# Kernel tuning notes

Measured on AMD Instinct MI355X. Metric: run time of the kernel, lower is better.

The kernel has to match this reference:

```python
import jax, jax.numpy as jnp
import numpy as np

B, CIN, H, W = 4, 256, 32, 32
COUT, DK, DV, NH = 256, 64, 64, 8
L = H * W
DKH = DK // NH
DVH = DV // NH
ALPHA, BETA = 0.5, 0.5
PAD = 1
LEAK = 0.01
GN_EPS = 1e-5


def conv2d(x, w, b=None, padding=0):
    out = jax.lax.conv_general_dilated(
        x, w, window_strides=(1, 1),
        padding=[(padding, padding), (padding, padding)],
        dimension_numbers=('NCHW', 'OIHW', 'NCHW'))
    if b is not None:
        out = out + b[None, :, None, None]
    return out


def rel_to_abs(x):
    # x: [B, Nh, L, 2L-1] -> [B, Nh, L, L]
    b, nh, l, _ = x.shape
    x = jnp.concatenate([x, jnp.zeros((b, nh, l, 1), x.dtype)], axis=3)
    flat = x.reshape(b, nh, l * 2 * l)
    flat = jnp.concatenate([flat, jnp.zeros((b, nh, l - 1), x.dtype)], axis=2)
    final = flat.reshape(b, nh, l + 1, 2 * l - 1)
    return final[:, :, :l, l - 1:]


def setup_inputs() -> dict:
    key = jax.random.key(0)
    ks = jax.random.split(key, 8)
    s = 0.02
    return {
        'x': jax.random.normal(ks[0], (B, CIN, H, W), jnp.float32),
        'prev_att': jax.random.normal(ks[1], (B, NH, L, L), jnp.float32) * 0.1,
        'conv_v': jax.random.normal(ks[2], (COUT - DV, CIN, 3, 3), jnp.float32) * s,
        'conv_g': jnp.ones((COUT - DV, 1, 1, 1), jnp.float32),
        'conv_b': jnp.zeros((COUT - DV,), jnp.float32),
        'qkv_w': jax.random.normal(ks[3], (2 * DK + DV, CIN, 1, 1), jnp.float32) * s,
        'qkv_b': jnp.zeros((2 * DK + DV,), jnp.float32),
        'attc_w': jax.random.normal(ks[4], (NH, NH, 3, 3), jnp.float32) * s,
        'attc_b': jnp.zeros((NH,), jnp.float32),
        'gn_w': jnp.ones((NH,), jnp.float32),
        'gn_b': jnp.zeros((NH,), jnp.float32),
        'rel_k': jax.random.normal(ks[5], (2 * L - 1, DKH), jnp.float32),
    }


def reference(x, prev_att, conv_v, conv_g, conv_b, qkv_w, qkv_b,
              attc_w, attc_b, gn_w, gn_b, rel_k):
    # ---- weight-normed conv branch (k < 1) ----
    vnorm = jnp.sqrt(jnp.sum(conv_v * conv_v, axis=(1, 2, 3), keepdims=True))
    w_eff = conv_g * conv_v / vnorm
    conv_out = conv2d(x, w_eff, conv_b, padding=PAD)
    conv_out = conv_out[:, :, :-PAD, :-PAD]  # Chomp2d

    # ---- attention branch (dk > 0, no downsample) ----
    qkv = conv2d(x, qkv_w, qkv_b, padding=0).reshape(B, 2 * DK + DV, L)
    q = qkv[:, :DK].reshape(B, NH, DKH, L) * (DKH ** -0.5)
    k = qkv[:, DK:2 * DK].reshape(B, NH, DKH, L)
    v = qkv[:, 2 * DK:].reshape(B, NH, DVH, L)

    logits = jnp.einsum('bhdl,bhdm->bhlm', q, k)  # [B,Nh,L,L]

    # relative position logits
    rel = jnp.einsum('bhld,md->bhlm', q.transpose(0, 1, 3, 2), rel_k)  # [B,Nh,L,2L-1]
    logits = logits + rel_to_abs(rel)

    # blend with previous attention + conv/GroupNorm refinement
    att_matrix = (1.0 - BETA) * logits + BETA * prev_att
    t = conv2d(att_matrix, attc_w, attc_b, padding=1)
    mu = jnp.mean(t, axis=(1, 2, 3), keepdims=True)
    var = jnp.var(t, axis=(1, 2, 3), keepdims=True)
    t = (t - mu) / jnp.sqrt(var + GN_EPS)
    t = t * gn_w[None, :, None, None] + gn_b[None, :, None, None]
    t = jnp.where(t >= 0, t, LEAK * t)  # LeakyReLU
    logits = ALPHA * t + (1.0 - ALPHA) * att_matrix

    weights = jax.nn.softmax(logits, axis=-1)
    attn = jnp.einsum('bhlm,bhmd->bhld', weights, v.transpose(0, 1, 3, 2))  # [B,Nh,L,dvh]
    # faithful to torch: reshape (not transpose) [B,Nh,L,dvh] -> [B,Nh,dvh,L]
    attn = attn.reshape(B, NH, DVH, L).reshape(B, DV, H, W)
    attn = attn[:, :, :-PAD, :-PAD]  # Chomp2d

    out = jnp.concatenate([conv_out, attn], axis=1)  # [B, COUT, H-1, W-1]
    return (out, logits)
```

## Files before the change

kernel.cpp:

```cpp
#include <hip/hip_runtime.h>
#include <math.h>

#define NB   4
#define CINc 256
#define LLEN 1024
#define NHEAD 8
#define QKVOC 192
#define CONVOC 192
#define OHW  31

#define WS_SCALE 0
#define WS_STATS 192
#define WS_PART  256
#define WS_QKV   8448
#define WS_E     794880
#define WS_CPART 1057024

typedef __attribute__((ext_vector_type(8))) short bf16x8;
typedef __attribute__((ext_vector_type(4))) float f32x4;

__device__ __forceinline__ unsigned short f2bf(float f) {
    unsigned int u = __float_as_uint(f);
    u += 0x7FFFu + ((u >> 16) & 1u);
    return (unsigned short)(u >> 16);
}
__device__ __forceinline__ float bf2f(unsigned short s) {
    return __uint_as_float(((unsigned int)s) << 16);
}

__global__ void k_wnorm(const float* __restrict__ conv_v, const float* __restrict__ conv_g,
                        float* __restrict__ ws) {
    int o = blockIdx.x, t = threadIdx.x;
    const float* v = conv_v + (size_t)o * 2304;
    float s = 0.f;
    for (int i = t; i < 2304; i += 256) { float x = v[i]; s += x * x; }
    for (int off = 1; off < 64; off <<= 1) s += __shfl_xor(s, off, 64);
    __shared__ float red[4];
    if ((t & 63) == 0) red[t >> 6] = s;
    __syncthreads();
    if (t == 0) {
        float tot = red[0] + red[1] + red[2] + red[3];
        ws[WS_SCALE + o] = conv_g[o] / sqrtf(tot);
    }
}

__global__ __launch_bounds__(256) void k_qkv(const float* __restrict__ x,
                                             const float* __restrict__ qkv_w,
                                             const float* __restrict__ qkv_b,
                                             float* __restrict__ ws) {
    int og = blockIdx.x, b = blockIdx.y, t = threadIdx.x;
    int o0 = og * 4;
    const float* xb = x + (size_t)b * CINc * LLEN;
    float acc[4][4] = {};
    for (int c = 0; c < CINc; c++) {
        float xv[4];
#pragma unroll
        for (int k = 0; k < 4; k++) xv[k] = xb[(size_t)c * LLEN + t + 256 * k];
#pragma unroll
        for (int oo = 0; oo < 4; oo++) {
            float w = qkv_w[(size_t)(o0 + oo) * CINc + c];
#pragma unroll
            for (int k = 0; k < 4; k++) acc[oo][k] += w * xv[k];
        }
    }
#pragma unroll
    for (int oo = 0; oo < 4; oo++) {
        int o = o0 + oo;
        float bias = qkv_b[o];
        float sc = (o < 64) ? 0.35355339059327373f : 1.0f;
#pragma unroll
        for (int k = 0; k < 4; k++)
            ws[WS_QKV + ((size_t)b * QKVOC + o) * LLEN + t + 256 * k] = (acc[oo][k] + bias) * sc;
    }
}

__global__ __launch_bounds__(256) void k_conv(const float* __restrict__ x,
                                              const float* __restrict__ conv_v,
                                              float* __restrict__ ws) {
    int ot = blockIdx.x, z = blockIdx.y, bz = blockIdx.z, t = threadIdx.x;
    int b = bz >> 1, half = bz & 1;
    int o0 = ot * 16, c0 = z * 32, r0 = half * 16;
    __shared__ unsigned short aW[16 * 288];
    __shared__ unsigned short xS[18 * 34 * 36];

    for (int idx = t; idx < 4608; idx += 256) {
        int o = idx / 288, k = idx - o * 288;
        int tap = k >> 5, c = k & 31;
        aW[o * 288 + k] = f2bf(conv_v[((size_t)(o0 + o) * CINc + c0 + c) * 9 + tap]);
    }
    unsigned int* xSu = reinterpret_cast<unsigned int*>(xS);
    for (int i = t; i < 11016; i += 256) xSu[i] = 0u;
    __syncthreads();
    const float* xb = x + ((size_t)b * CINc + c0) * 1024;
    for (int task = t; task < 2304; task += 256) {
        int cp = task & 15;
        int rr = (task >> 4) % 18;
        int wc = task / 288;
        int gr = r0 - 1 + rr;
        int gw = wc * 4;
        if (gr >= 0 && gr < 32) {
            float4 va = *reinterpret_cast<const float4*>(&xb[(size_t)(2 * cp) * 1024 + gr * 32 + gw]);
            float4 vb = *reinterpret_cast<const float4*>(&xb[(size_t)(2 * cp + 1) * 1024 + gr * 32 + gw]);
            int base = (rr * 34 + gw + 1) * 36 + 2 * cp;
            float a0[4] = {va.x, va.y, va.z, va.w};
            float b0[4] = {vb.x, vb.y, vb.z, vb.w};
#pragma unroll
            for (int j = 0; j < 4; j++) {
                unsigned int pk = (unsigned int)f2bf(a0[j]) | ((unsigned int)f2bf(b0[j]) << 16);
                *reinterpret_cast<unsigned int*>(&xS[base + j * 36]) = pk;
            }
        }
    }
    __syncthreads();

    int lane = t & 63, w = t >> 6;
    int col = lane & 15, kb = lane >> 4;
    bf16x8 afr[9];
#pragma unroll
    for (int tap = 0; tap < 9; tap++)
        afr[tap] = *reinterpret_cast<const bf16x8*>(&aW[col * 288 + tap * 32 + kb * 8]);
    char* xb8 = reinterpret_cast<char*>(xS);
#pragma unroll
    for (int tt = 0; tt < 8; tt++) {
        int pt = w * 8 + tt;
        int hl = pt >> 1, w0 = (pt & 1) * 16;
        f32x4 acc = {0.f, 0.f, 0.f, 0.f};
        int pbase = (hl * 34 + w0 + col) * 72 + kb * 16;
#pragma unroll
        for (int tap = 0; tap < 9; tap++) {
            int di = tap / 3, dj = tap % 3;
            bf16x8 bfr = *reinterpret_cast<const bf16x8*>(xb8 + pbase + (di * 34 + dj) * 72);
            acc = __builtin_amdgcn_mfma_f32_16x16x32_bf16(afr[tap], bfr, acc, 0, 0, 0);
        }
        int px = (r0 + hl) * 32 + w0 + col;
#pragma unroll
        for (int r = 0; r < 4; r++) {
            int o = kb * 4 + r;
            ws[WS_CPART + ((size_t)(b * 8 + z) * CONVOC + o0 + o) * 1024 + px] = acc[r];
        }
    }
}

__global__ __launch_bounds__(256) void k_convred(const float* __restrict__ conv_b,
                                                 const float* __restrict__ ws,
                                                 float* __restrict__ out) {
    int o = blockIdx.x, b = blockIdx.y, t = threadIdx.x;
    float sc = ws[WS_SCALE + o], bi = conv_b[o];
    for (int px = t; px < 1024; px += 256) {
        float s = 0.f;
#pragma unroll
        for (int z = 0; z < 8; z++)
            s += ws[WS_CPART + ((size_t)(b * 8 + z) * CONVOC + o) * 1024 + px];
        int hh = px >> 5, ww = px & 31;
        if (hh < 31 && ww < 31)
            out[((size_t)(b * 256 + o) * 31 + hh) * 31 + ww] = sc * s + bi;
    }
}

__global__ __launch_bounds__(256, 3) void k_att(const float* __restrict__ ws_,
                                                const float* __restrict__ prev,
                                                const float* __restrict__ rel_k,
                                                unsigned short* __restrict__ attB) {
    int jt = blockIdx.x, it = blockIdx.y, bh = blockIdx.z;
    int b = bh >> 3, h = bh & 7;
    int t = threadIdx.x;
    int i0 = it * 32, j0 = jt * 128;
    int ig = t >> 5, tj = t & 31;

    float4 pv[4];
    size_t poff = (((size_t)bh * 1024 + i0 + ig * 4) << 10) + j0 + tj * 4;
#pragma unroll
    for (int ii = 0; ii < 4; ii++)
        pv[ii] = *reinterpret_cast<const float4*>(&prev[poff + ((size_t)ii << 10)]);
    const float* rbase = rel_k + (size_t)(j0 - i0 + 1020 + 4 * (tj - ig)) * 8;
    float4 ra[7], rb[7];
#pragma unroll
    for (int dgi = 0; dgi < 7; dgi++) {
        ra[dgi] = *reinterpret_cast<const float4*>(rbase + dgi * 8);
        rb[dgi] = *reinterpret_cast<const float4*>(rbase + dgi * 8 + 4);
    }

    __shared__ float kS[8][128];
    __shared__ float qS[32][8];
    const float* qkv = ws_ + WS_QKV;
    const float* qplane = qkv + ((size_t)b * QKVOC + h * 8) * LLEN;
    const float* kplane = qkv + ((size_t)b * QKVOC + 64 + h * 8) * LLEN;
    {
        int d = t >> 5, jc = (t & 31) * 4;
        *reinterpret_cast<float4*>(&kS[d][jc]) =
            *reinterpret_cast<const float4*>(&kplane[(size_t)d * LLEN + j0 + jc]);
    }
    {
        int i = t >> 3, d = t & 7;
        qS[i][d] = qplane[(size_t)d * LLEN + i0 + i];
    }
    __syncthreads();

    float qr[4][8];
#pragma unroll
    for (int ii = 0; ii < 4; ii++) {
        float4 a = *reinterpret_cast<const float4*>(&qS[ig * 4 + ii][0]);
        float4 c = *reinterpret_cast<const float4*>(&qS[ig * 4 + ii][4]);
        qr[ii][0] = a.x; qr[ii][1] = a.y; qr[ii][2] = a.z; qr[ii][3] = a.w;
        qr[ii][4] = c.x; qr[ii][5] = c.y; qr[ii][6] = c.z; qr[ii][7] = c.w;
    }
    float acc[4][4] = {};
#pragma unroll
    for (int d = 0; d < 8; d++) {
        float4 kv = *reinterpret_cast<const float4*>(&kS[d][tj * 4]);
#pragma unroll
        for (int ii = 0; ii < 4; ii++) {
            float qv = qr[ii][d];
            acc[ii][0] += qv * kv.x; acc[ii][1] += qv * kv.y;
            acc[ii][2] += qv * kv.z; acc[ii][3] += qv * kv.w;
        }
    }
#pragma unroll
    for (int dgi = 0; dgi < 7; dgi++) {
#pragma unroll
        for (int ii = 0; ii < 4; ii++) {
#pragma unroll
            for (int jj = 0; jj < 4; jj++) {
                if (jj - ii + 3 == dgi) {
                    acc[ii][jj] += qr[ii][0] * ra[dgi].x + qr[ii][1] * ra[dgi].y
                                 + qr[ii][2] * ra[dgi].z + qr[ii][3] * ra[dgi].w
                                 + qr[ii][4] * rb[dgi].x + qr[ii][5] * rb[dgi].y
                                 + qr[ii][6] * rb[dgi].z + qr[ii][7] * rb[dgi].w;
                }
            }
        }
    }
#pragma unroll
    for (int ii = 0; ii < 4; ii++) {
        int i = i0 + ig * 4 + ii;
        size_t off = (((size_t)bh * 1024 + i) << 10) + j0 + tj * 4;
        ushort4 o16;
        o16.x = f2bf(0.5f * acc[ii][0] + 0.5f * pv[ii].x);
        o16.y = f2bf(0.5f * acc[ii][1] + 0.5f * pv[ii].y);
        o16.z = f2bf(0.5f * acc[ii][2] + 0.5f * pv[ii].z);
        o16.w = f2bf(0.5f * acc[ii][3] + 0.5f * pv[ii].w);
        *reinterpret_cast<ushort4*>(&attB[off]) = o16;
    }
}

__global__ __launch_bounds__(256) void k_attconv(const unsigned short* __restrict__ attB,
                                                 const float* __restrict__ attc_w,
                                                 const float* __restrict__ attc_b,
                                                 unsigned short* __restrict__ tB,
                                                 float* __restrict__ ws) {
    int jt = blockIdx.x, it = blockIdx.y, b = blockIdx.z, t = threadIdx.x;
    int i0 = it * 16, j0 = jt * 64;
    __shared__ unsigned short aW[16 * 96];
    __shared__ unsigned short xT[18 * 81 * 8];
    unsigned int* xU = reinterpret_cast<unsigned int*>(xT);

    for (int idx = t; idx < 1536; idx += 256) {
        int ho = idx / 96, k = idx - ho * 96;
        int tap = k >> 3, hp = k & 7;
        float w = (ho < 8 && tap < 9) ? attc_w[ho * 72 + hp * 9 + tap] : 0.f;
        aW[ho * 96 + k] = f2bf(w);
    }
    const unsigned short* attb = attB + (((size_t)b * 8) << 20);
    for (int task = t; task < 720; task += 256) {
        int r   = task % 18;
        int hpp = (task / 18) & 3;
        int ch  = task / 72;
        int gr  = i0 - 1 + r;
        int gc0 = j0 - 8 + ch * 8;
        uint4 va = make_uint4(0u, 0u, 0u, 0u), vb = va;
        if (gr >= 0 && gr < 1024 && gc0 >= 0 && gc0 < 1024) {
            size_t base = (((size_t)(hpp * 2)) << 20) + ((size_t)gr << 10) + gc0;
            va = *reinterpret_cast<const uint4*>(&attb[base]);
            vb = *reinterpret_cast<const uint4*>(&attb[base + (1u << 20)]);
        }
        int cbase = (r * 81 + ch * 8) * 4 + hpp;
        unsigned int aw[4] = {va.x, va.y, va.z, va.w};
        unsigned int bw[4] = {vb.x, vb.y, vb.z, vb.w};
#pragma unroll
        for (int q = 0; q < 4; q++) {
            xU[cbase + (2 * q) * 4]     = (aw[q] & 0xffffu) | (bw[q] << 16);
            xU[cbase + (2 * q + 1) * 4] = (aw[q] >> 16) | (bw[q] & 0xffff0000u);
        }
    }
    __syncthreads();

    int lane = t & 63, w = t >> 6;
    int col = lane & 15, kb = lane >> 4;
    bf16x8 afr[3];
#pragma unroll
    for (int c = 0; c < 3; c++)
        afr[c] = *reinterpret_cast<const bf16x8*>(&aW[col * 96 + c * 32 + kb * 8]);
    int offs[3];
#pragma unroll
    for (int c = 0; c < 3; c++) {
        int tap = c * 4 + kb;
        int di = (tap < 9) ? tap / 3 : 1;
        int dj = (tap < 9) ? tap % 3 : 1;
        offs[c] = (di * 81 + col + dj + 7) * 16;
    }
    float bias_r[4];
#pragma unroll
    for (int r = 0; r < 4; r++) {
        int ho = kb * 4 + r;
        bias_r[r] = (ho < 8) ? attc_b[ho] : 0.f;
    }
    float ssum = 0.f, ssq = 0.f;
    char* xbyte = reinterpret_cast<char*>(xT);
#pragma unroll
    for (int ri = 0; ri < 4; ri++) {
        int il = w * 4 + ri;
#pragma unroll
        for (int jg = 0; jg < 4; jg++) {
            f32x4 acc = {0.f, 0.f, 0.f, 0.f};
            int base = (il * 81 + jg * 16) * 16;
#pragma unroll
            for (int c = 0; c < 3; c++) {
                bf16x8 bfr = *reinterpret_cast<const bf16x8*>(xbyte + base + offs[c]);
                acc = __builtin_amdgcn_mfma_f32_16x16x32_bf16(afr[c], bfr, acc, 0, 0, 0);
            }
#pragma unroll
            for (int r = 0; r < 4; r++) {
                float v = acc[r] + bias_r[r];
                ssum += v; ssq += v * v;
                int ho = kb * 4 + r;
                if (ho < 8) {
                    size_t off = (((size_t)(b * 8 + ho)) << 20) + ((size_t)(i0 + il) << 10)
                               + j0 + jg * 16 + col;
                    tB[off] = f2bf(v);
                }
            }
        }
    }
    for (int off = 1; off < 64; off <<= 1) {
        ssum += __shfl_xor(ssum, off, 64);
        ssq  += __shfl_xor(ssq, off, 64);
    }
    __shared__ float r1[4], r2[4];
    if ((t & 63) == 0) { r1[t >> 6] = ssum; r2[t >> 6] = ssq; }
    __syncthreads();
    if (t == 0) {
        int lin = (b * 64 + it) * 16 + jt;
        ws[WS_PART + lin * 2]     = r1[0] + r1[1] + r1[2] + r1[3];
        ws[WS_PART + lin * 2 + 1] = r2[0] + r2[1] + r2[2] + r2[3];
    }
}

__global__ void k_stats(float* __restrict__ ws) {
    int b = blockIdx.x, t = threadIdx.x;
    float S = 0.f, Q = 0.f;
    for (int n = t; n < 1024; n += 256) {
        S += ws[WS_PART + (size_t)(b * 1024 + n) * 2];
        Q += ws[WS_PART + (size_t)(b * 1024 + n) * 2 + 1];
    }
    for (int off = 1; off < 64; off <<= 1) { S += __shfl_xor(S, off, 64); Q += __shfl_xor(Q, off, 64); }
    __shared__ float r1[4], r2[4];
    if ((t & 63) == 0) { r1[t >> 6] = S; r2[t >> 6] = Q; }
    __syncthreads();
    if (t == 0) {
        float Sa = r1[0] + r1[1] + r1[2] + r1[3];
        float Qa = r2[0] + r2[1] + r2[2] + r2[3];
        float N = 8.0f * 1024.f * 1024.f;
        float mean = Sa / N;
        float var = Qa / N - mean * mean;
        ws[WS_STATS + b * 2]     = mean;
        ws[WS_STATS + b * 2 + 1] = 1.0f / sqrtf(var + 1e-5f);
    }
}

__global__ __launch_bounds__(256) void k_final(const unsigned short* __restrict__ tB,
                                               const unsigned short* __restrict__ attB,
                                               float* __restrict__ logits,
                                               const float* __restrict__ gn_w,
                                               const float* __restrict__ gn_b,
                                               float* __restrict__ ws) {
    int row0 = blockIdx.x * 4;
    int b = row0 >> 13, h = (row0 >> 10) & 7;
    int t = threadIdx.x;
    float mean = ws[WS_STATS + b * 2], rstd = ws[WS_STATS + b * 2 + 1];
    float gwr = gn_w[h] * rstd;
    float gbm = gn_b[h] - mean * gwr;
    __shared__ float p[4][1024];
    __shared__ float red2[4][4];
    size_t base = (size_t)row0 * 1024 + t * 4;
    ushort4 tv[4], av[4];
#pragma unroll
    for (int r = 0; r < 4; r++) {
        tv[r] = *reinterpret_cast<const ushort4*>(&tB[base + (size_t)r * 1024]);
        av[r] = *reinterpret_cast<const ushort4*>(&attB[base + (size_t)r * 1024]);
    }
    float s[4];
#pragma unroll
    for (int r = 0; r < 4; r++) {
        float tt[4] = {bf2f(tv[r].x), bf2f(tv[r].y), bf2f(tv[r].z), bf2f(tv[r].w)};
        float aa[4] = {bf2f(av[r].x), bf2f(av[r].y), bf2f(av[r].z), bf2f(av[r].w)};
        float lg[4], e[4];
#pragma unroll
        for (int k = 0; k < 4; k++) {
            float xv = tt[k] * gwr + gbm;
            xv = fmaxf(xv, 0.01f * xv);
            lg[k] = 0.5f * xv + 0.5f * aa[k];
            e[k] = __expf(lg[k]);
        }
        *reinterpret_cast<float4*>(&logits[base + (size_t)r * 1024]) =
            make_float4(lg[0], lg[1], lg[2], lg[3]);
        *reinterpret_cast<float4*>(&p[r][t * 4]) = make_float4(e[0], e[1], e[2], e[3]);
        s[r] = (e[0] + e[1]) + (e[2] + e[3]);
    }
#pragma unroll
    for (int off = 1; off < 64; off <<= 1) {
#pragma unroll
        for (int r = 0; r < 4; r++) s[r] += __shfl_xor(s[r], off, 64);
    }
    int wvi = t >> 6, ln = t & 63;
    if (ln == 0) {
#pragma unroll
        for (int r = 0; r < 4; r++) red2[wvi][r] = s[r];
    }
    __syncthreads();
    float sr[4];
#pragma unroll
    for (int r = 0; r < 4; r++)
        sr[r] = (red2[0][r] + red2[1][r]) + (red2[2][r] + red2[3][r]);
    int d = t >> 5, c = t & 31;
    const float* vrow = ws + WS_QKV + ((size_t)b * QKVOC + 128 + h * 8 + d) * LLEN;
    float a[4] = {0.f, 0.f, 0.f, 0.f};
#pragma unroll
    for (int u = 0; u < 8; u++) {
        int j = 4 * c + 128 * u;
        float4 vv = *reinterpret_cast<const float4*>(&vrow[j]);
#pragma unroll
        for (int r = 0; r < 4; r++) {
            float4 pv = *reinterpret_cast<const float4*>(&p[r][j]);
            a[r] += pv.x * vv.x + pv.y * vv.y + pv.z * vv.z + pv.w * vv.w;
        }
    }
#pragma unroll
    for (int off = 1; off < 32; off <<= 1) {
#pragma unroll
        for (int r = 0; r < 4; r++) a[r] += __shfl_xor(a[r], off, 64);
    }
    if (c == 0) {
#pragma unroll
        for (int r = 0; r < 4; r++)
            ws[WS_E + (size_t)(row0 + r) * 8 + d] = a[r] / sr[r];
    }
}

__global__ void k_scatter(const float* __restrict__ ws, float* __restrict__ out) {
    int idx = blockIdx.x * 256 + threadIdx.x;
    if (idx >= 4 * 64 * 31 * 31) return;
    int x = idx % 31; int rest = idx / 31;
    int y = rest % 31; rest /= 31;
    int hd = rest % 64; int b = rest / 64;
    int h = hd >> 3, d = hd & 7;
    int flat = d * 1024 + y * 32 + x;
    int lp = flat >> 3, mp = flat & 7;
    float v = ws[WS_E + ((size_t)(b * 8 + h) * 1024 + lp) * 8 + mp];
    out[((size_t)(b * 256 + 192 + hd) * 31 + y) * 31 + x] = v;
}

extern "C" void kernel_launch(void* const* d_in, const int* in_sizes, int n_in,
                              void* d_out, int out_size, void* d_ws, size_t ws_size,
                              hipStream_t stream) {
    (void)in_sizes; (void)n_in; (void)out_size; (void)ws_size;
    const float* x      = (const float*)d_in[0];
    const float* prev   = (const float*)d_in[1];
    const float* conv_v = (const float*)d_in[2];
    const float* conv_g = (const float*)d_in[3];
    const float* conv_b = (const float*)d_in[4];
    const float* qkv_w  = (const float*)d_in[5];
    const float* qkv_b  = (const float*)d_in[6];
    const float* attc_w = (const float*)d_in[7];
    const float* attc_b = (const float*)d_in[8];
    const float* gn_w   = (const float*)d_in[9];
    const float* gn_b   = (const float*)d_in[10];
    const float* rel_k  = (const float*)d_in[11];
    float* out = (float*)d_out;
    float* ws  = (float*)d_ws;
    float* logits = out + 984064;
    unsigned short* attB = (unsigned short*)(ws + 1057024);
    unsigned short* tB   = attB + 33554432;

    k_wnorm<<<192, 256, 0, stream>>>(conv_v, conv_g, ws);
    k_qkv<<<dim3(48, 4), 256, 0, stream>>>(x, qkv_w, qkv_b, ws);
    k_conv<<<dim3(12, 8, 8), 256, 0, stream>>>(x, conv_v, ws);
    k_convred<<<dim3(192, 4), 256, 0, stream>>>(conv_b, ws, out);
    k_att<<<dim3(8, 32, 32), 256, 0, stream>>>(ws, prev, rel_k, attB);
    k_attconv<<<dim3(16, 64, 4), 256, 0, stream>>>(attB, attc_w, attc_b, tB, ws);
    k_stats<<<4, 256, 0, stream>>>(ws);
    k_final<<<8192, 256, 0, stream>>>(tB, attB, logits, gn_w, gn_b, ws);
    k_scatter<<<961, 256, 0, stream>>>(ws, out);
}
```

Measured before the change: 276.8 us.

## Loop k_att over column tiles with double-buffered K and prefetched prev_att

Each k_att block now processes a full 1024-column row strip in eight 128-wide steps instead of one tile, reusing the loaded Q registers across steps. K tiles are double-buffered in shared memory and the next tile's K and prev_att values are prefetched into registers while the current tile is computed. This cuts the grid from 8192 to 1024 blocks and adds more registers and a per-step barrier, which may lower occupancy and parallelism.

```diff
diff --git a/kernel.cpp b/kernel.cpp
--- a/kernel.cpp
+++ b/kernel.cpp
@@ -161,39 +161,31 @@
                                                 const float* __restrict__ prev,
                                                 const float* __restrict__ rel_k,
                                                 unsigned short* __restrict__ attB) {
-    int jt = blockIdx.x, it = blockIdx.y, bh = blockIdx.z;
+    int it = blockIdx.x, bh = blockIdx.y;
     int b = bh >> 3, h = bh & 7;
     int t = threadIdx.x;
-    int i0 = it * 32, j0 = jt * 128;
+    int i0 = it * 32;
     int ig = t >> 5, tj = t & 31;
 
-    float4 pv[4];
-    size_t poff = (((size_t)bh * 1024 + i0 + ig * 4) << 10) + j0 + tj * 4;
-#pragma unroll
-    for (int ii = 0; ii < 4; ii++)
-        pv[ii] = *reinterpret_cast<const float4*>(&prev[poff + ((size_t)ii << 10)]);
-    const float* rbase = rel_k + (size_t)(j0 - i0 + 1020 + 4 * (tj - ig)) * 8;
-    float4 ra[7], rb[7];
-#pragma unroll
-    for (int dgi = 0; dgi < 7; dgi++) {
-        ra[dgi] = *reinterpret_cast<const float4*>(rbase + dgi * 8);
-        rb[dgi] = *reinterpret_cast<const float4*>(rbase + dgi * 8 + 4);
-    }
-
-    __shared__ float kS[8][128];
+    __shared__ float kS[2][8][128];
     __shared__ float qS[32][8];
     const float* qkv = ws_ + WS_QKV;
     const float* qplane = qkv + ((size_t)b * QKVOC + h * 8) * LLEN;
     const float* kplane = qkv + ((size_t)b * QKVOC + 64 + h * 8) * LLEN;
-    {
-        int d = t >> 5, jc = (t & 31) * 4;
-        *reinterpret_cast<float4*>(&kS[d][jc]) =
-            *reinterpret_cast<const float4*>(&kplane[(size_t)d * LLEN + j0 + jc]);
-    }
+
+    int kd = t >> 5, kjc = (t & 31) * 4;
+    size_t prow = ((size_t)bh * 1024 + i0 + ig * 4) << 10;
+
     {
         int i = t >> 3, d = t & 7;
         qS[i][d] = qplane[(size_t)d * LLEN + i0 + i];
     }
+    float4 kreg = *reinterpret_cast<const float4*>(&kplane[(size_t)kd * LLEN + kjc]);
+    float4 pvbuf[4];
+#pragma unroll
+    for (int ii = 0; ii < 4; ii++)
+        pvbuf[ii] = *reinterpret_cast<const float4*>(&prev[prow + ((size_t)ii << 10) + tj * 4]);
+    *reinterpret_cast<float4*>(&kS[0][kd][kjc]) = kreg;
     __syncthreads();
 
     float qr[4][8];
@@ -204,42 +196,71 @@
         qr[ii][0] = a.x; qr[ii][1] = a.y; qr[ii][2] = a.z; qr[ii][3] = a.w;
         qr[ii][4] = c.x; qr[ii][5] = c.y; qr[ii][6] = c.z; qr[ii][7] = c.w;
     }
-    float acc[4][4] = {};
-#pragma unroll
-    for (int d = 0; d < 8; d++) {
-        float4 kv = *reinterpret_cast<const float4*>(&kS[d][tj * 4]);
-#pragma unroll
-        for (int ii = 0; ii < 4; ii++) {
-            float qv = qr[ii][d];
-            acc[ii][0] += qv * kv.x; acc[ii][1] += qv * kv.y;
-            acc[ii][2] += qv * kv.z; acc[ii][3] += qv * kv.w;
-        }
-    }
-#pragma unroll
-    for (int dgi = 0; dgi < 7; dgi++) {
-#pragma unroll
-        for (int ii = 0; ii < 4; ii++) {
-#pragma unroll
-            for (int jj = 0; jj < 4; jj++) {
-                if (jj - ii + 3 == dgi) {
-                    acc[ii][jj] += qr[ii][0] * ra[dgi].x + qr[ii][1] * ra[dgi].y
-                                 + qr[ii][2] * ra[dgi].z + qr[ii][3] * ra[dgi].w
-                                 + qr[ii][4] * rb[dgi].x + qr[ii][5] * rb[dgi].y
-                                 + qr[ii][6] * rb[dgi].z + qr[ii][7] * rb[dgi].w;
+
+    int cur = 0;
+#pragma unroll 1
+    for (int u = 0; u < 8; u++) {
+        int j0 = u * 128;
+        bool more = (u < 7);
+        float4 kregn = make_float4(0.f, 0.f, 0.f, 0.f);
+        float4 pvn[4];
+        if (more) {
+            kregn = *reinterpret_cast<const float4*>(&kplane[(size_t)kd * LLEN + j0 + 128 + kjc]);
+#pragma unroll
+            for (int ii = 0; ii < 4; ii++)
+                pvn[ii] = *reinterpret_cast<const float4*>(
+                    &prev[prow + ((size_t)ii << 10) + j0 + 128 + tj * 4]);
+        }
+        const float* rbase = rel_k + (size_t)(j0 - i0 + 1020 + 4 * (tj - ig)) * 8;
+        float4 ra[7], rb[7];
+#pragma unroll
+        for (int dgi = 0; dgi < 7; dgi++) {
+            ra[dgi] = *reinterpret_cast<const float4*>(rbase + dgi * 8);
+            rb[dgi] = *reinterpret_cast<const float4*>(rbase + dgi * 8 + 4);
+        }
+        float acc[4][4] = {};
+#pragma unroll
+        for (int d = 0; d < 8; d++) {
+            float4 kv = *reinterpret_cast<const float4*>(&kS[cur][d][tj * 4]);
+#pragma unroll
+            for (int ii = 0; ii < 4; ii++) {
+                float qv = qr[ii][d];
+                acc[ii][0] += qv * kv.x; acc[ii][1] += qv * kv.y;
+                acc[ii][2] += qv * kv.z; acc[ii][3] += qv * kv.w;
+            }
+        }
+#pragma unroll
+        for (int dgi = 0; dgi < 7; dgi++) {
+#pragma unroll
+            for (int ii = 0; ii < 4; ii++) {
+#pragma unroll
+                for (int jj = 0; jj < 4; jj++) {
+                    if (jj - ii + 3 == dgi) {
+                        acc[ii][jj] += qr[ii][0] * ra[dgi].x + qr[ii][1] * ra[dgi].y
+                                     + qr[ii][2] * ra[dgi].z + qr[ii][3] * ra[dgi].w
+                                     + qr[ii][4] * rb[dgi].x + qr[ii][5] * rb[dgi].y
+                                     + qr[ii][6] * rb[dgi].z + qr[ii][7] * rb[dgi].w;
+                    }
                 }
             }
         }
-    }
-#pragma unroll
-    for (int ii = 0; ii < 4; ii++) {
-        int i = i0 + ig * 4 + ii;
-        size_t off = (((size_t)bh * 1024 + i) << 10) + j0 + tj * 4;
-        ushort4 o16;
-        o16.x = f2bf(0.5f * acc[ii][0] + 0.5f * pv[ii].x);
-        o16.y = f2bf(0.5f * acc[ii][1] + 0.5f * pv[ii].y);
-        o16.z = f2bf(0.5f * acc[ii][2] + 0.5f * pv[ii].z);
-        o16.w = f2bf(0.5f * acc[ii][3] + 0.5f * pv[ii].w);
-        *reinterpret_cast<ushort4*>(&attB[off]) = o16;
+#pragma unroll
+        for (int ii = 0; ii < 4; ii++) {
+            size_t off = prow + ((size_t)ii << 10) + j0 + tj * 4;
+            ushort4 o16;
+            o16.x = f2bf(0.5f * acc[ii][0] + 0.5f * pvbuf[ii].x);
+            o16.y = f2bf(0.5f * acc[ii][1] + 0.5f * pvbuf[ii].y);
+            o16.z = f2bf(0.5f * acc[ii][2] + 0.5f * pvbuf[ii].z);
+            o16.w = f2bf(0.5f * acc[ii][3] + 0.5f * pvbuf[ii].w);
+            *reinterpret_cast<ushort4*>(&attB[off]) = o16;
+        }
+        if (more) {
+            *reinterpret_cast<float4*>(&kS[cur ^ 1][kd][kjc]) = kregn;
+#pragma unroll
+            for (int ii = 0; ii < 4; ii++) pvbuf[ii] = pvn[ii];
+            cur ^= 1;
+            __syncthreads();
+        }
     }
 }
 
@@ -485,7 +506,7 @@
     k_qkv<<<dim3(48, 4), 256, 0, stream>>>(x, qkv_w, qkv_b, ws);
     k_conv<<<dim3(12, 8, 8), 256, 0, stream>>>(x, conv_v, ws);
     k_convred<<<dim3(192, 4), 256, 0, stream>>>(conv_b, ws, out);
-    k_att<<<dim3(8, 32, 32), 256, 0, stream>>>(ws, prev, rel_k, attB);
+    k_att<<<dim3(32, 32), 256, 0, stream>>>(ws, prev, rel_k, attB);
     k_attconv<<<dim3(16, 64, 4), 256, 0, stream>>>(attB, attc_w, attc_b, tB, ws);
     k_stats<<<4, 256, 0, stream>>>(ws);
     k_final<<<8192, 256, 0, stream>>>(tB, attB, logits, gn_w, gn_b, ws);
```

Result: slower. 439.2 us (+58.7%).
